# Kernel optimization log

Hardware: AMD Instinct MI355X
Metric: run time of the kernel (lower is better)

Reference implementation:

```python
import jax, jax.numpy as jnp
from jax import lax
import numpy as np

B, T, I, H = 4096, 200, 32, 6  # batch, seq_len, input_size, hidden


def _lstm_layer(x_seq, W_ih, W_hh, b_ih, b_hh):
    """Single unidirectional LSTM layer, PyTorch gate order (i,f,g,o).
    x_seq: [B,T,Din]. Returns (all_h [B,T,H], h_last [B,H])."""
    Bb = x_seq.shape[0]
    Hh = W_hh.shape[1]
    # Precompute input projections for all timesteps (hoisted out of the scan).
    x_proj = jnp.einsum('bti,gi->btg', x_seq, W_ih) + b_ih + b_hh  # [B,T,4H]

    def step(carry, xp_t):
        h, c = carry
        gates = xp_t + h @ W_hh.T  # [B,4H]
        i_g, f_g, g_g, o_g = jnp.split(gates, 4, axis=-1)
        i_g = jax.nn.sigmoid(i_g)
        f_g = jax.nn.sigmoid(f_g)
        g_g = jnp.tanh(g_g)
        o_g = jax.nn.sigmoid(o_g)
        c = f_g * c + i_g * g_g
        h = o_g * jnp.tanh(c)
        return (h, c), h

    init = (jnp.zeros((Bb, Hh), x_seq.dtype), jnp.zeros((Bb, Hh), x_seq.dtype))
    (h_last, _), hs = lax.scan(step, init, jnp.swapaxes(x_proj, 0, 1))  # time-major scan
    return jnp.swapaxes(hs, 0, 1), h_last


def setup_inputs() -> dict:
    key = jax.random.key(0)
    ks = jax.random.split(key, 11)
    s = 0.2  # ~ uniform(-1/sqrt(H)) scale for H=6
    inp = {
        'x': jax.random.normal(ks[0], (B, T, I), dtype=jnp.float32),
        'W_ih0': jax.random.normal(ks[1], (4 * H, I), dtype=jnp.float32) * s,
        'W_hh0': jax.random.normal(ks[2], (4 * H, H), dtype=jnp.float32) * s,
        'b_ih0': jax.random.normal(ks[3], (4 * H,), dtype=jnp.float32) * s,
        'b_hh0': jax.random.normal(ks[4], (4 * H,), dtype=jnp.float32) * s,
        'W_ih1': jax.random.normal(ks[5], (4 * H, H), dtype=jnp.float32) * s,
        'W_hh1': jax.random.normal(ks[6], (4 * H, H), dtype=jnp.float32) * s,
        'b_ih1': jax.random.normal(ks[7], (4 * H,), dtype=jnp.float32) * s,
        'b_hh1': jax.random.normal(ks[8], (4 * H,), dtype=jnp.float32) * s,
        'W_lin': jax.random.normal(ks[9], (1, H), dtype=jnp.float32) * s,
        'b_lin': jax.random.normal(ks[10], (1,), dtype=jnp.float32) * s,
    }
    return inp


def reference(x, W_ih0, W_hh0, b_ih0, b_hh0, W_ih1, W_hh1, b_ih1, b_hh1, W_lin, b_lin):
    # Layer 0 (eval mode: inter-layer dropout disabled)
    h1_seq, _ = _lstm_layer(x, W_ih0, W_hh0, b_ih0, b_hh0)
    # Layer 1
    _, h2_last = _lstm_layer(h1_seq, W_ih1, W_hh1, b_ih1, b_hh1)
    # Linear head on last layer's final hidden state: [B,1]
    return h2_last @ W_lin.T + b_lin
```

## Files before the change

### kernel.cpp

```cpp
#include <hip/hip_runtime.h>


#define TLEN  200
#define ISZ   32
#define HSZ   6
#define WPITCH 36

#define PWOFF 0
#define PBOFF (24 * WPITCH)
#define PLDS_DW (PBOFF + 24)

#define RPITCH 25
#define RING_DW (64 * RPITCH)
#define FWOFF  RING_DW
#define FBOFF  (FWOFF + 24 * WPITCH)
#define FLDS_DW (FBOFF + 24)

#define XP4_COUNT ((size_t)4096 * TLEN * 6)
#define WS_REQ    ((XP4_COUNT + 6) * 16)

__device__ __forceinline__ float fast_sig(float x) {
    return __builtin_amdgcn_rcpf(1.0f + __expf(-x));
}
__device__ __forceinline__ float tanh_s(float x) {
    return fmaf(2.0f, fast_sig(x + x), -1.0f);
}
__device__ __forceinline__ float rl(float v, int l) {
    return __int_as_float(__builtin_amdgcn_readlane(__float_as_int(v), l));
}
template <int CTRL>
__device__ __forceinline__ float qperm(float v) {
    return __int_as_float(__builtin_amdgcn_mov_dpp(__float_as_int(v), CTRL, 0xf, 0xf, true));
}
template <int OFF>
__device__ __forceinline__ float swz(float v) {
    return __int_as_float(__builtin_amdgcn_ds_swizzle(__float_as_int(v), OFF));
}
__device__ __forceinline__ float dot4(float4 w, float4 v) {
    return fmaf(w.x, v.x, fmaf(w.y, v.y, fmaf(w.z, v.z, w.w * v.w)));
}

__global__ __launch_bounds__(64) void proj_k(
    const float* __restrict__ x,    const float* __restrict__ Wih0,
    const float* __restrict__ bih0, const float* __restrict__ bhh0,
    const float* __restrict__ bih1, const float* __restrict__ bhh1,
    float4* __restrict__ xp4)
{
    __shared__ float lds[PLDS_DW];
    const int lane = threadIdx.x;
    const int b    = blockIdx.x;
    const int o = lane & 1;
    const int L = lane >> 1;
    const float* xb = x + (size_t)b * TLEN * ISZ;

#pragma unroll
    for (int k = 0; k < 13; ++k) {
        const int idx = lane + (k << 6);
        if (idx < 768) {
            const int row = idx >> 5, kk = idx & 31;
            const int slot = ((row % 6) / 3) * 12 + (row / 6) * 3 + (row % 3);
            lds[PWOFF + slot * WPITCH + kk] = Wih0[idx];
        } else if (idx < 792) {
            const int r = idx - 768;
            const int slot = ((r % 6) / 3) * 12 + (r / 6) * 3 + (r % 3);
            lds[PBOFF + slot] = bih0[r] + bhh0[r];
        }
    }
    if (blockIdx.x == 0 && lane < 24) {
        const int u = lane % 6, g = lane / 6;
        ((float*)(xp4 + XP4_COUNT))[u * 4 + g] = bih1[g * 6 + u] + bhh1[g * 6 + u];
    }

#define PLDSW(ROW, KCQ) (*(const float4*)&lds[PWOFF + (o * 12 + (ROW)) * WPITCH + ((KCQ) << 2)])
#pragma unroll 1
    for (int w = 0; w < 7; ++w) {
        const int t = (w << 5) + L;
        if (t < TLEN) {
            const float4* xr4 = (const float4*)(xb + (size_t)t * ISZ);
            float a0c[12];
#pragma unroll
            for (int jj = 0; jj < 12; ++jj) a0c[jj] = 0.0f;
#pragma unroll
            for (int hh = 0; hh < 2; ++hh) {
                float4 xw[4];
#pragma unroll
                for (int q = 0; q < 4; ++q) xw[q] = xr4[(hh << 2) + q];
#pragma unroll
                for (int jh = 0; jh < 2; ++jh)
#pragma unroll
                    for (int kc = 0; kc < 4; ++kc)
#pragma unroll
                        for (int jj = jh * 6; jj < jh * 6 + 6; ++jj)
                            a0c[jj] += dot4(PLDSW(jj, (hh << 2) + kc), xw[kc]);
            }
            float vv[12];
#pragma unroll
            for (int jj = 0; jj < 12; ++jj) vv[jj] = a0c[jj] + lds[PBOFF + o * 12 + jj];
            float4* dst = xp4 + ((size_t)b * TLEN + t) * 6 + 3 * o;
#pragma unroll
            for (int v = 0; v < 3; ++v)
                dst[v] = make_float4(vv[v], vv[3 + v], vv[6 + v], vv[9 + v]);
        }
    }
#undef PLDSW
}

__global__ __launch_bounds__(64) void lstm_scan(
    const float* __restrict__ Whh0, const float* __restrict__ Wih1,
    const float* __restrict__ Whh1, const float* __restrict__ Wlin,
    const float* __restrict__ blin, const float4* __restrict__ xp4,
    float* __restrict__ out)
{
    const int lane = threadIdx.x;
    const int role = lane & 15;
    const int grp  = lane >> 4;
    const int b    = blockIdx.x * 4 + grp;

    float WA[4][6], WB[4][6];
#pragma unroll
    for (int g = 0; g < 4; ++g)
#pragma unroll
        for (int k = 0; k < 6; ++k) { WA[g][k] = 0.0f; WB[g][k] = 0.0f; }
    if (role < 6) {
#pragma unroll
        for (int g = 0; g < 4; ++g)
#pragma unroll
            for (int k = 0; k < 6; ++k) WA[g][k] = Whh0[(g * 6 + role) * 6 + k];
    } else if (role < 12) {
        const int u = role - 6;
#pragma unroll
        for (int g = 0; g < 4; ++g)
#pragma unroll
            for (int k = 0; k < 6; ++k) {
                WA[g][k] = Wih1[(g * 6 + u) * 6 + k];
                WB[g][k] = Whh1[(g * 6 + u) * 6 + k];
            }
    }
    const float4* P;
    int ST;
    if (role < 6) { P = xp4 + (size_t)b * TLEN * 6 + role; ST = 6; }
    else          { P = xp4 + XP4_COUNT + (role < 12 ? role - 6 : 0); ST = 0; }

    float4 q0 = P[0], q1 = P[ST], q2 = P[2 * ST], q3 = P[3 * ST];
    P += 4 * ST;

    float c = 0.0f, h = 0.0f;

#define STEP(XQ) do { \
    const float hA0 = swz<0x010>(h), hA1 = swz<0x030>(h), hA2 = swz<0x050>(h); \
    const float hA3 = swz<0x070>(h), hA4 = swz<0x090>(h), hA5 = swz<0x0B0>(h); \
    const float hB0 = swz<0x0D0>(h), hB1 = swz<0x0F0>(h), hB2 = swz<0x110>(h); \
    const float hB3 = swz<0x130>(h), hB4 = swz<0x150>(h), hB5 = swz<0x170>(h); \
    float a0 = (XQ).x, a1 = (XQ).y, a2 = (XQ).z, a3 = (XQ).w; \
    ARG(a0, 0); ARG(a1, 1); ARG(a2, 2); ARG(a3, 3); \
    const float ig = fast_sig(a0), fg = fast_sig(a1); \
    const float gg = tanh_s(a2),   og = fast_sig(a3); \
    c = fmaf(fg, c, ig * gg); \
    h = og * tanh_s(c); \
} while (0)

#define ARG(A, G) do { \
    const float s0 = fmaf(WA[G][0], hA0, fmaf(WA[G][1], hA1, fmaf(WA[G][2], hA2, A))); \
    const float s1 = fmaf(WA[G][3], hA3, fmaf(WA[G][4], hA4, WA[G][5] * hA5)); \
    const float s2 = fmaf(WB[G][0], hB0, fmaf(WB[G][1], hB1, WB[G][2] * hB2)); \
    const float s3 = fmaf(WB[G][3], hB3, fmaf(WB[G][4], hB4, WB[G][5] * hB5)); \
    A = (s0 + s1) + (s2 + s3); \
} while (0)

#define STEPR(QV) do { const float4 _xq = QV; QV = *P; P += ST; STEP(_xq); } while (0)

    STEPR(q0);
    h = (role < 6) ? h : 0.0f;
    c = (role < 6) ? c : 0.0f;

#pragma unroll 1
    for (int m = 0; m < 48; ++m) {
        STEPR(q1); STEPR(q2); STEPR(q3); STEPR(q0);
    }
    STEPR(q1); STEPR(q2); STEPR(q3);
    STEP(q0); STEP(q1); STEP(q2); STEP(q3);
    STEP(q0);

    {
        const float f0 = swz<0x0D0>(h), f1 = swz<0x0F0>(h), f2 = swz<0x110>(h);
        const float f3 = swz<0x130>(h), f4 = swz<0x150>(h), f5 = swz<0x170>(h);
        float s = blin[0];
        s = fmaf(Wlin[0], f0, s); s = fmaf(Wlin[1], f1, s);
        s = fmaf(Wlin[2], f2, s); s = fmaf(Wlin[3], f3, s);
        s = fmaf(Wlin[4], f4, s); s = fmaf(Wlin[5], f5, s);
        if (role == 0) out[b] = s;
    }
#undef STEP
#undef ARG
#undef STEPR
}

__global__ __launch_bounds__(64) void lstm_fb(
    const float* __restrict__ x,
    const float* __restrict__ Wih0, const float* __restrict__ Whh0,
    const float* __restrict__ bih0, const float* __restrict__ bhh0,
    const float* __restrict__ Wih1, const float* __restrict__ Whh1,
    const float* __restrict__ bih1, const float* __restrict__ bhh1,
    const float* __restrict__ Wlin, const float* __restrict__ blin,
    float* __restrict__ out)
{
    __shared__ float lds[FLDS_DW];

    const int lane = threadIdx.x;
    const int b    = blockIdx.x;

    const int o = lane & 1;
    const int L = lane >> 1;

    const bool loHalf = (lane < 32);
    const int  p  = lane & 3;
    const int  jq = (lane & 31) >> 2;
    const int  j  = (jq < HSZ) ? jq : 0;
    const int  r  = 6 * p + j;

#define LDSW(ROW, KCQ) (*(const float4*)&lds[FWOFF + (o * 12 + (ROW)) * WPITCH + ((KCQ) << 2)])

#pragma unroll
    for (int k = 0; k < 13; ++k) {
        const int idx = lane + (k << 6);
        if (idx < 768) {
            const int row = idx >> 5, kk = idx & 31;
            lds[FWOFF + row * WPITCH + kk] = Wih0[idx];
        } else if (idx < 792) {
            lds[FBOFF + idx - 768] = bih0[idx - 768] + bhh0[idx - 768];
        }
    }

    float WA[6], WB[6], base1 = 0.0f, sgc = 1.0f, tgc = 0.0f;
#pragma unroll
    for (int k = 0; k < 6; ++k) { WA[k] = 0.0f; WB[k] = 0.0f; }
    if (loHalf) {
#pragma unroll
        for (int k = 0; k < 6; ++k) WA[k] = Whh0[r * 6 + k];
    } else {
#pragma unroll
        for (int k = 0; k < 6; ++k) { WA[k] = Wih1[r * 6 + k]; WB[k] = Whh1[r * 6 + k]; }
        base1 = bih1[r] + bhh1[r];
    }
    if (p == 2) {
#pragma unroll
        for (int k = 0; k < 6; ++k) { WA[k] *= 2.0f; WB[k] *= 2.0f; }
        base1 *= 2.0f; sgc = 2.0f; tgc = -1.0f;
    }

    const float* xb = x + (size_t)b * TLEN * ISZ;

#pragma unroll
    for (int w01 = 0; w01 < 2; ++w01) {
        const int t = (w01 << 5) + L;
        const float4* xr4 = (const float4*)(xb + t * ISZ);
        float4 xw[8];
#pragma unroll
        for (int q = 0; q < 8; ++q) xw[q] = xr4[q];
        float a0c[12];
#pragma unroll
        for (int jj = 0; jj < 12; ++jj) a0c[jj] = 0.0f;
#pragma unroll
        for (int kc = 0; kc < 8; ++kc)
#pragma unroll
            for (int jj = 0; jj < 12; ++jj)
                a0c[jj] += dot4(LDSW(jj, kc), xw[kc]);
#pragma unroll
        for (int jj = 0; jj < 12; ++jj) {
            float v = a0c[jj] + lds[FBOFF + o * 12 + jj];
            if (jj < 6) v = (o == 1) ? v * 2.0f : v;
            lds[t * RPITCH + o * 12 + jj] = v;
        }
    }

    float acc[12];
#pragma unroll
    for (int jj = 0; jj < 12; ++jj) acc[jj] = 0.0f;
    const float* pc = xb + (size_t)min(64 + L, TLEN - 1) * ISZ;
    const float* pn = xb + (size_t)min(96 + L, TLEN - 1) * ISZ;
    float4 f0, f1;
    f1 = *((const float4*)pc);
    float4 Wp0 = LDSW(0, 0), Wp1 = LDSW(1, 0), Wp2 = LDSW(2, 0);

    float c = 0.0f, h = 0.0f;
    float xp_cur = lds[r];

#define KC_HEAD(KC) do { \
    f0 = f1; \
    const float4* _srcp = ((KC) < 7) ? ((const float4*)pc + (KC) + 1) \
                                     : ((const float4*)pn); \
    f1 = *_srcp; \
} while (0)

#define SPREAD_STEP(RT, KC) do { \
    acc[3*(RT)+0] += dot4(Wp0, f0); \
    acc[3*(RT)+1] += dot4(Wp1, f0); \
    acc[3*(RT)+2] += dot4(Wp2, f0); \
    const int _rtn = ((RT) + 1) & 3; \
    const int _kcn = ((RT) == 3) ? (((KC) + 1) & 7) : (KC); \
    Wp0 = LDSW(3*_rtn + 0, _kcn); \
    Wp1 = LDSW(3*_rtn + 1, _kcn); \
    Wp2 = LDSW(3*_rtn + 2, _kcn); \
} while (0)

#define SCAN_STEP(ITV) do { \
    const float h10=rl(h,0),  h11=rl(h,4),  h12=rl(h,8); \
    const float h13=rl(h,12), h14=rl(h,16), h15=rl(h,20); \
    const float h20=rl(h,32), h21=rl(h,36), h22=rl(h,40); \
    const float h23=rl(h,44), h24=rl(h,48), h25=rl(h,52); \
    const float _xn = lds[(((ITV) + 1) & 63) * RPITCH + r]; \
    const float _g0 = loHalf ? xp_cur : base1; \
    const float _a0 = fmaf(WA[0],h10, fmaf(WA[2],h12, fmaf(WA[4],h14, _g0))); \
    const float _a1 = fmaf(WA[1],h11, fmaf(WA[3],h13, WA[5]*h15)); \
    const float _b0 = fmaf(WB[0],h20, fmaf(WB[2],h22, WB[4]*h24)); \
    const float _b1 = fmaf(WB[1],h21, fmaf(WB[3],h23, WB[5]*h25)); \
    const float _g  = (_a0 + _a1) + (_b0 + _b1); \
    const float _aG = fmaf(sgc, fast_sig(_g), tgc); \
    const float _iq = qperm<0x00>(_aG), _fq = qperm<0x55>(_aG); \
    const float _gq = qperm<0xAA>(_aG), _oq = qperm<0xFF>(_aG); \
    c = fmaf(_fq, c, _iq * _gq); \
    const float _th = fmaf(2.0f, fast_sig(2.0f * c), -1.0f); \
    h = _oq * _th; \
    xp_cur = _xn; \
    if ((ITV) == 200) { \
        float _s = blin[0]; \
        _s = fmaf(Wlin[0], rl(h, 32), _s); \
        _s = fmaf(Wlin[1], rl(h, 36), _s); \
        _s = fmaf(Wlin[2], rl(h, 40), _s); \
        _s = fmaf(Wlin[3], rl(h, 44), _s); \
        _s = fmaf(Wlin[4], rl(h, 48), _s); \
        _s = fmaf(Wlin[5], rl(h, 52), _s); \
        if (lane == 0) out[b] = _s; \
    } \
} while (0)

#define ENTRY(IT0) do { \
    const int _slot = ((IT0) + 32 + L) & 63; \
    _Pragma("unroll") \
    for (int _jj = 0; _jj < 12; ++_jj) { \
        float _v = acc[_jj] + lds[FBOFF + o * 12 + _jj]; \
        if (_jj < 6) _v = (o == 1) ? _v * 2.0f : _v; \
        lds[_slot * RPITCH + o * 12 + _jj] = _v; \
        acc[_jj] = 0.0f; \
    } \
    pc = pn; \
    pn = xb + (size_t)min((IT0) + 96 + L, TLEN - 1) * ISZ; \
} while (0)

    KC_HEAD(0);
    SPREAD_STEP(0, 0);
    {
        const float g  = loHalf ? xp_cur : base1;
        const float aG = fmaf(sgc, fast_sig(g), tgc);
        const float iq = qperm<0x00>(aG), gq = qperm<0xAA>(aG), oq = qperm<0xFF>(aG);
        const float cn = iq * gq;
        const float th = fmaf(2.0f, fast_sig(2.0f * cn), -1.0f);
        c = loHalf ? cn : 0.0f;
        h = loHalf ? (oq * th) : 0.0f;
        xp_cur = lds[RPITCH + r];
    }

    SPREAD_STEP(1, 0); SCAN_STEP(1);
    SPREAD_STEP(2, 0); SCAN_STEP(2);
    SPREAD_STEP(3, 0); SCAN_STEP(3);
    for (int kc = 1; kc < 8; ++kc) {
        KC_HEAD(kc);
        const int itb = kc << 2;
        SPREAD_STEP(0, kc); SCAN_STEP(itb + 0);
        SPREAD_STEP(1, kc); SCAN_STEP(itb + 1);
        SPREAD_STEP(2, kc); SCAN_STEP(itb + 2);
        SPREAD_STEP(3, kc); SCAN_STEP(itb + 3);
    }

    for (int w = 1; w < 7; ++w) {
        const int it0 = w << 5;
        ENTRY(it0);
        for (int kc = 0; kc < 8; ++kc) {
            const int itb = it0 + (kc << 2);
            if (itb > 200) break;
            KC_HEAD(kc);
            SPREAD_STEP(0, kc); SCAN_STEP(itb + 0);
            SPREAD_STEP(1, kc); SCAN_STEP(itb + 1);
            SPREAD_STEP(2, kc); SCAN_STEP(itb + 2);
            SPREAD_STEP(3, kc); SCAN_STEP(itb + 3);
        }
    }

#undef LDSW
#undef KC_HEAD
#undef SPREAD_STEP
#undef SCAN_STEP
#undef ENTRY
}

extern "C" void kernel_launch(void* const* d_in, const int* in_sizes, int n_in,
                              void* d_out, int out_size, void* d_ws, size_t ws_size,
                              hipStream_t stream) {
    const float* x    = (const float*)d_in[0];
    const float* Wih0 = (const float*)d_in[1];
    const float* Whh0 = (const float*)d_in[2];
    const float* bih0 = (const float*)d_in[3];
    const float* bhh0 = (const float*)d_in[4];
    const float* Wih1 = (const float*)d_in[5];
    const float* Whh1 = (const float*)d_in[6];
    const float* bih1 = (const float*)d_in[7];
    const float* bhh1 = (const float*)d_in[8];
    const float* Wlin = (const float*)d_in[9];
    const float* blin = (const float*)d_in[10];
    float* out = (float*)d_out;

    if (d_ws != nullptr && ws_size >= WS_REQ) {
        float4* xp4 = (float4*)d_ws;
        proj_k<<<4096, 64, 0, stream>>>(x, Wih0, bih0, bhh0, bih1, bhh1, xp4);
        lstm_scan<<<1024, 64, 0, stream>>>(Whh0, Wih1, Whh1, Wlin, blin,
                                           (const float4*)xp4, out);
    } else {
        lstm_fb<<<4096, 64, 0, stream>>>(x, Wih0, Whh0, bih0, bhh0,
                                         Wih1, Whh1, bih1, bhh1,
                                         Wlin, blin, out);
    }
}
```

Measured before the change: 253.2 us.

## Flatten projection to one row per thread; use DPP row rotates in scan

The input projection kernel now gives each thread a single (batch,time) row, with weights read straight from global/constant memory instead of an LDS-staged layout, over 12800 blocks. The scan kernel swaps the 12 ds_swizzle broadcasts per step for 15 DPP row-rotates, with weights pre-permuted per lane so each lane does 16 FMAs per gate. The aim is to cut LDS-path latency on the serial recurrence and simplify projection scheduling. The cost is more FMAs per step and heavier register use, and the projection now relies on scalar weight loads.

```diff
diff --git a/kernel.cpp b/kernel.cpp
--- a/kernel.cpp
+++ b/kernel.cpp
@@ -5,10 +5,6 @@
 #define ISZ   32
 #define HSZ   6
 #define WPITCH 36
-
-#define PWOFF 0
-#define PBOFF (24 * WPITCH)
-#define PLDS_DW (PBOFF + 24)
 
 #define RPITCH 25
 #define RING_DW (64 * RPITCH)
@@ -36,76 +32,54 @@
 __device__ __forceinline__ float swz(float v) {
     return __int_as_float(__builtin_amdgcn_ds_swizzle(__float_as_int(v), OFF));
 }
+template <int M>
+__device__ __forceinline__ float rotf(float v) {
+    return __int_as_float(__builtin_amdgcn_mov_dpp(__float_as_int(v), 0x120 + M, 0xf, 0xf, true));
+}
 __device__ __forceinline__ float dot4(float4 w, float4 v) {
     return fmaf(w.x, v.x, fmaf(w.y, v.y, fmaf(w.z, v.z, w.w * v.w)));
 }
 
-__global__ __launch_bounds__(64) void proj_k(
+__global__ __launch_bounds__(64) void proj_k2(
     const float* __restrict__ x,    const float* __restrict__ Wih0,
     const float* __restrict__ bih0, const float* __restrict__ bhh0,
     const float* __restrict__ bih1, const float* __restrict__ bhh1,
     float4* __restrict__ xp4)
 {
-    __shared__ float lds[PLDS_DW];
     const int lane = threadIdx.x;
-    const int b    = blockIdx.x;
-    const int o = lane & 1;
-    const int L = lane >> 1;
-    const float* xb = x + (size_t)b * TLEN * ISZ;
-
-#pragma unroll
-    for (int k = 0; k < 13; ++k) {
-        const int idx = lane + (k << 6);
-        if (idx < 768) {
-            const int row = idx >> 5, kk = idx & 31;
-            const int slot = ((row % 6) / 3) * 12 + (row / 6) * 3 + (row % 3);
-            lds[PWOFF + slot * WPITCH + kk] = Wih0[idx];
-        } else if (idx < 792) {
-            const int r = idx - 768;
-            const int slot = ((r % 6) / 3) * 12 + (r / 6) * 3 + (r % 3);
-            lds[PBOFF + slot] = bih0[r] + bhh0[r];
-        }
-    }
+    const size_t n = (size_t)blockIdx.x * 64 + lane;
+
     if (blockIdx.x == 0 && lane < 24) {
         const int u = lane % 6, g = lane / 6;
         ((float*)(xp4 + XP4_COUNT))[u * 4 + g] = bih1[g * 6 + u] + bhh1[g * 6 + u];
     }
 
-#define PLDSW(ROW, KCQ) (*(const float4*)&lds[PWOFF + (o * 12 + (ROW)) * WPITCH + ((KCQ) << 2)])
-#pragma unroll 1
-    for (int w = 0; w < 7; ++w) {
-        const int t = (w << 5) + L;
-        if (t < TLEN) {
-            const float4* xr4 = (const float4*)(xb + (size_t)t * ISZ);
-            float a0c[12];
-#pragma unroll
-            for (int jj = 0; jj < 12; ++jj) a0c[jj] = 0.0f;
-#pragma unroll
-            for (int hh = 0; hh < 2; ++hh) {
-                float4 xw[4];
-#pragma unroll
-                for (int q = 0; q < 4; ++q) xw[q] = xr4[(hh << 2) + q];
-#pragma unroll
-                for (int jh = 0; jh < 2; ++jh)
-#pragma unroll
-                    for (int kc = 0; kc < 4; ++kc)
-#pragma unroll
-                        for (int jj = jh * 6; jj < jh * 6 + 6; ++jj)
-                            a0c[jj] += dot4(PLDSW(jj, (hh << 2) + kc), xw[kc]);
-            }
-            float vv[12];
-#pragma unroll
-            for (int jj = 0; jj < 12; ++jj) vv[jj] = a0c[jj] + lds[PBOFF + o * 12 + jj];
-            float4* dst = xp4 + ((size_t)b * TLEN + t) * 6 + 3 * o;
-#pragma unroll
-            for (int v = 0; v < 3; ++v)
-                dst[v] = make_float4(vv[v], vv[3 + v], vv[6 + v], vv[9 + v]);
+    const float4* xr = (const float4*)(x + n * ISZ);
+    float4 xv[8];
+#pragma unroll
+    for (int q = 0; q < 8; ++q) xv[q] = xr[q];
+
+    float acc[24];
+#pragma unroll
+    for (int r = 0; r < 24; ++r) {
+        float a = bih0[r] + bhh0[r];
+        const float* wr = Wih0 + r * ISZ;
+#pragma unroll
+        for (int q = 0; q < 8; ++q) {
+            a = fmaf(wr[q * 4 + 0], xv[q].x, a);
+            a = fmaf(wr[q * 4 + 1], xv[q].y, a);
+            a = fmaf(wr[q * 4 + 2], xv[q].z, a);
+            a = fmaf(wr[q * 4 + 3], xv[q].w, a);
         }
-    }
-#undef PLDSW
-}
-
-__global__ __launch_bounds__(64) void lstm_scan(
+        acc[r] = a;
+    }
+    float4* dst = xp4 + n * 6;
+#pragma unroll
+    for (int u = 0; u < 6; ++u)
+        dst[u] = make_float4(acc[u], acc[6 + u], acc[12 + u], acc[18 + u]);
+}
+
+__global__ __launch_bounds__(64) void scan_k3(
     const float* __restrict__ Whh0, const float* __restrict__ Wih1,
     const float* __restrict__ Whh1, const float* __restrict__ Wlin,
     const float* __restrict__ blin, const float4* __restrict__ xp4,
@@ -116,26 +90,31 @@
     const int grp  = lane >> 4;
     const int b    = blockIdx.x * 4 + grp;
 
-    float WA[4][6], WB[4][6];
+    int sr[16];
+    sr[0] = role;
+#define PRB(M) sr[M] = __builtin_amdgcn_mov_dpp(lane, 0x120 + M, 0xf, 0xf, true) & 15;
+    PRB(1)  PRB(2)  PRB(3)  PRB(4)  PRB(5)  PRB(6)  PRB(7)
+    PRB(8)  PRB(9)  PRB(10) PRB(11) PRB(12) PRB(13) PRB(14) PRB(15)
+#undef PRB
+
+    const int lt = (role < 6) ? 0 : (role < 12 ? 1 : 2);
+    const int u  = (role < 6) ? role : (role < 12 ? role - 6 : 0);
+    float Wq[4][16];
 #pragma unroll
     for (int g = 0; g < 4; ++g)
 #pragma unroll
-        for (int k = 0; k < 6; ++k) { WA[g][k] = 0.0f; WB[g][k] = 0.0f; }
-    if (role < 6) {
-#pragma unroll
-        for (int g = 0; g < 4; ++g)
-#pragma unroll
-            for (int k = 0; k < 6; ++k) WA[g][k] = Whh0[(g * 6 + role) * 6 + k];
-    } else if (role < 12) {
-        const int u = role - 6;
-#pragma unroll
-        for (int g = 0; g < 4; ++g)
-#pragma unroll
-            for (int k = 0; k < 6; ++k) {
-                WA[g][k] = Wih1[(g * 6 + u) * 6 + k];
-                WB[g][k] = Whh1[(g * 6 + u) * 6 + k];
+        for (int m = 0; m < 16; ++m) {
+            const int s = sr[m];
+            float w = 0.0f;
+            if (lt == 0) {
+                if (s < 6) w = Whh0[(g * 6 + u) * 6 + s];
+            } else if (lt == 1) {
+                if (s < 6)       w = Wih1[(g * 6 + u) * 6 + s];
+                else if (s < 12) w = Whh1[(g * 6 + u) * 6 + (s - 6)];
             }
-    }
+            Wq[g][m] = w;
+        }
+
     const float4* P;
     int ST;
     if (role < 6) { P = xp4 + (size_t)b * TLEN * 6 + role; ST = 6; }
@@ -146,25 +125,38 @@
 
     float c = 0.0f, h = 0.0f;
 
+#define GATE(G, BASE) ({ \
+    float _s0 = fmaf(Wq[G][0], h, (BASE)); \
+    _s0 = fmaf(Wq[G][2],  hm2,  _s0); \
+    _s0 = fmaf(Wq[G][4],  hm4,  _s0); \
+    _s0 = fmaf(Wq[G][6],  hm6,  _s0); \
+    _s0 = fmaf(Wq[G][8],  hm8,  _s0); \
+    _s0 = fmaf(Wq[G][10], hm10, _s0); \
+    _s0 = fmaf(Wq[G][12], hm12, _s0); \
+    _s0 = fmaf(Wq[G][14], hm14, _s0); \
+    float _s1 = fmaf(Wq[G][1], hm1, Wq[G][3] * hm3); \
+    _s1 = fmaf(Wq[G][5],  hm5,  _s1); \
+    _s1 = fmaf(Wq[G][7],  hm7,  _s1); \
+    _s1 = fmaf(Wq[G][9],  hm9,  _s1); \
+    _s1 = fmaf(Wq[G][11], hm11, _s1); \
+    _s1 = fmaf(Wq[G][13], hm13, _s1); \
+    _s1 = fmaf(Wq[G][15], hm15, _s1); \
+    _s0 + _s1; })
+
 #define STEP(XQ) do { \
-    const float hA0 = swz<0x010>(h), hA1 = swz<0x030>(h), hA2 = swz<0x050>(h); \
-    const float hA3 = swz<0x070>(h), hA4 = swz<0x090>(h), hA5 = swz<0x0B0>(h); \
-    const float hB0 = swz<0x0D0>(h), hB1 = swz<0x0F0>(h), hB2 = swz<0x110>(h); \
-    const float hB3 = swz<0x130>(h), hB4 = swz<0x150>(h), hB5 = swz<0x170>(h); \
-    float a0 = (XQ).x, a1 = (XQ).y, a2 = (XQ).z, a3 = (XQ).w; \
-    ARG(a0, 0); ARG(a1, 1); ARG(a2, 2); ARG(a3, 3); \
-    const float ig = fast_sig(a0), fg = fast_sig(a1); \
-    const float gg = tanh_s(a2),   og = fast_sig(a3); \
+    const float hm1 = rotf<1>(h),   hm2 = rotf<2>(h),   hm3 = rotf<3>(h); \
+    const float hm4 = rotf<4>(h),   hm5 = rotf<5>(h),   hm6 = rotf<6>(h); \
+    const float hm7 = rotf<7>(h),   hm8 = rotf<8>(h),   hm9 = rotf<9>(h); \
+    const float hm10 = rotf<10>(h), hm11 = rotf<11>(h), hm12 = rotf<12>(h); \
+    const float hm13 = rotf<13>(h), hm14 = rotf<14>(h), hm15 = rotf<15>(h); \
+    const float A0 = GATE(0, (XQ).x); \
+    const float A1 = GATE(1, (XQ).y); \
+    const float A2 = GATE(2, (XQ).z); \
+    const float A3 = GATE(3, (XQ).w); \
+    const float ig = fast_sig(A0), fg = fast_sig(A1); \
+    const float gg = tanh_s(A2),   og = fast_sig(A3); \
     c = fmaf(fg, c, ig * gg); \
     h = og * tanh_s(c); \
-} while (0)
-
-#define ARG(A, G) do { \
-    const float s0 = fmaf(WA[G][0], hA0, fmaf(WA[G][1], hA1, fmaf(WA[G][2], hA2, A))); \
-    const float s1 = fmaf(WA[G][3], hA3, fmaf(WA[G][4], hA4, WA[G][5] * hA5)); \
-    const float s2 = fmaf(WB[G][0], hB0, fmaf(WB[G][1], hB1, WB[G][2] * hB2)); \
-    const float s3 = fmaf(WB[G][3], hB3, fmaf(WB[G][4], hB4, WB[G][5] * hB5)); \
-    A = (s0 + s1) + (s2 + s3); \
 } while (0)
 
 #define STEPR(QV) do { const float4 _xq = QV; QV = *P; P += ST; STEP(_xq); } while (0)
@@ -191,8 +183,8 @@
         if (role == 0) out[b] = s;
     }
 #undef STEP
-#undef ARG
 #undef STEPR
+#undef GATE
 }
 
 __global__ __launch_bounds__(64) void lstm_fb(
@@ -411,9 +403,9 @@
 
     if (d_ws != nullptr && ws_size >= WS_REQ) {
         float4* xp4 = (float4*)d_ws;
-        proj_k<<<4096, 64, 0, stream>>>(x, Wih0, bih0, bhh0, bih1, bhh1, xp4);
-        lstm_scan<<<1024, 64, 0, stream>>>(Whh0, Wih1, Whh1, Wlin, blin,
-                                           (const float4*)xp4, out);
+        proj_k2<<<12800, 64, 0, stream>>>(x, Wih0, bih0, bhh0, bih1, bhh1, xp4);
+        scan_k3<<<1024, 64, 0, stream>>>(Whh0, Wih1, Whh1, Wlin, blin,
+                                         (const float4*)xp4, out);
     } else {
         lstm_fb<<<4096, 64, 0, stream>>>(x, Wih0, Whh0, bih0, bhh0,
                                          Wih1, Whh1, bih1, bhh1,
```

After: 291.3 us. 15.1% more time.

## Restructure projection kernel per-gate with LDS-staged x, halve scan batches per wave

Applied to the files above, without the earlier changes.

The projection kernel now assigns one gate row per lane and keeps its 32 input weights in registers. It stages 64 timesteps of x into LDS and has two lane groups handle alternating timesteps, writing scalar outputs in the interleaved layout. This replaces the old version, which read weights from LDS and had each lane compute 12 gates. The scan kernel now packs only 2 batch elements per 64-lane wave instead of 4 and launches twice as many blocks, aiming for more waves and latency hiding at the cost of half-idle lanes. The projection stores become scattered 4-byte writes, and a quarter of its lanes do no work.

```diff
diff --git a/kernel.cpp b/kernel.cpp
--- a/kernel.cpp
+++ b/kernel.cpp
@@ -5,10 +5,6 @@
 #define ISZ   32
 #define HSZ   6
 #define WPITCH 36
-
-#define PWOFF 0
-#define PBOFF (24 * WPITCH)
-#define PLDS_DW (PBOFF + 24)
 
 #define RPITCH 25
 #define RING_DW (64 * RPITCH)
@@ -40,72 +36,69 @@
     return fmaf(w.x, v.x, fmaf(w.y, v.y, fmaf(w.z, v.z, w.w * v.w)));
 }
 
-__global__ __launch_bounds__(64) void proj_k(
+__global__ __launch_bounds__(64) void proj_k3(
     const float* __restrict__ x,    const float* __restrict__ Wih0,
     const float* __restrict__ bih0, const float* __restrict__ bhh0,
     const float* __restrict__ bih1, const float* __restrict__ bhh1,
     float4* __restrict__ xp4)
 {
-    __shared__ float lds[PLDS_DW];
+    __shared__ float xs[64 * 36];
+
     const int lane = threadIdx.x;
     const int b    = blockIdx.x;
-    const int o = lane & 1;
-    const int L = lane >> 1;
     const float* xb = x + (size_t)b * TLEN * ISZ;
 
-#pragma unroll
-    for (int k = 0; k < 13; ++k) {
-        const int idx = lane + (k << 6);
-        if (idx < 768) {
-            const int row = idx >> 5, kk = idx & 31;
-            const int slot = ((row % 6) / 3) * 12 + (row / 6) * 3 + (row % 3);
-            lds[PWOFF + slot * WPITCH + kk] = Wih0[idx];
-        } else if (idx < 792) {
-            const int r = idx - 768;
-            const int slot = ((r % 6) / 3) * 12 + (r / 6) * 3 + (r % 3);
-            lds[PBOFF + slot] = bih0[r] + bhh0[r];
-        }
-    }
-    if (blockIdx.x == 0 && lane < 24) {
+    if (b == 0 && lane < 24) {
         const int u = lane % 6, g = lane / 6;
         ((float*)(xp4 + XP4_COUNT))[u * 4 + g] = bih1[g * 6 + u] + bhh1[g * 6 + u];
     }
 
-#define PLDSW(ROW, KCQ) (*(const float4*)&lds[PWOFF + (o * 12 + (ROW)) * WPITCH + ((KCQ) << 2)])
+    const int s  = lane / 24;
+    const int se = (s == 2) ? 0 : s;
+    const int g  = lane - s * 24;
+    const bool act = (lane < 48);
+
+    float4 w4[8];
+    const float4* wr = (const float4*)(Wih0 + g * ISZ);
+#pragma unroll
+    for (int q = 0; q < 8; ++q) w4[q] = wr[q];
+    const float bg = bih0[g] + bhh0[g];
+
+    const int ofs = (g % 6) * 4 + g / 6;
+    float* xpb = (float*)(xp4 + (size_t)b * TLEN * 6);
+
 #pragma unroll 1
-    for (int w = 0; w < 7; ++w) {
-        const int t = (w << 5) + L;
-        if (t < TLEN) {
-            const float4* xr4 = (const float4*)(xb + (size_t)t * ISZ);
-            float a0c[12];
-#pragma unroll
-            for (int jj = 0; jj < 12; ++jj) a0c[jj] = 0.0f;
-#pragma unroll
-            for (int hh = 0; hh < 2; ++hh) {
-                float4 xw[4];
-#pragma unroll
-                for (int q = 0; q < 4; ++q) xw[q] = xr4[(hh << 2) + q];
-#pragma unroll
-                for (int jh = 0; jh < 2; ++jh)
-#pragma unroll
-                    for (int kc = 0; kc < 4; ++kc)
-#pragma unroll
-                        for (int jj = jh * 6; jj < jh * 6 + 6; ++jj)
-                            a0c[jj] += dot4(PLDSW(jj, (hh << 2) + kc), xw[kc]);
+    for (int tc = 0; tc < TLEN; tc += 64) {
+        const int nrows = (TLEN - tc >= 64) ? 64 : (TLEN - tc);
+        const float4* src = (const float4*)(xb + (size_t)tc * ISZ);
+        for (int f = lane; f < nrows * 8; f += 64) {
+            const int row = f >> 3, kq = f & 7;
+            *(float4*)&xs[row * 36 + kq * 4] = src[f];
+        }
+        const int half = nrows >> 1;
+#pragma unroll 1
+        for (int i = 0; i < half; ++i) {
+            const int rr = 2 * i + se;
+            float a0 = bg, a1 = 0.0f;
+#pragma unroll
+            for (int q = 0; q < 4; ++q) {
+                const float4 xv = *(const float4*)&xs[rr * 36 + q * 4];
+                a0 = fmaf(w4[q].x, xv.x, a0); a0 = fmaf(w4[q].y, xv.y, a0);
+                a0 = fmaf(w4[q].z, xv.z, a0); a0 = fmaf(w4[q].w, xv.w, a0);
             }
-            float vv[12];
-#pragma unroll
-            for (int jj = 0; jj < 12; ++jj) vv[jj] = a0c[jj] + lds[PBOFF + o * 12 + jj];
-            float4* dst = xp4 + ((size_t)b * TLEN + t) * 6 + 3 * o;
-#pragma unroll
-            for (int v = 0; v < 3; ++v)
-                dst[v] = make_float4(vv[v], vv[3 + v], vv[6 + v], vv[9 + v]);
+#pragma unroll
+            for (int q = 4; q < 8; ++q) {
+                const float4 xv = *(const float4*)&xs[rr * 36 + q * 4];
+                a1 = fmaf(w4[q].x, xv.x, a1); a1 = fmaf(w4[q].y, xv.y, a1);
+                a1 = fmaf(w4[q].z, xv.z, a1); a1 = fmaf(w4[q].w, xv.w, a1);
+            }
+            const float a = a0 + a1;
+            if (act) xpb[(size_t)(tc + rr) * 24 + ofs] = a;
         }
     }
-#undef PLDSW
-}
-
-__global__ __launch_bounds__(64) void lstm_scan(
+}
+
+__global__ __launch_bounds__(64) void scan_k4(
     const float* __restrict__ Whh0, const float* __restrict__ Wih1,
     const float* __restrict__ Whh1, const float* __restrict__ Wlin,
     const float* __restrict__ blin, const float4* __restrict__ xp4,
@@ -114,37 +107,47 @@
     const int lane = threadIdx.x;
     const int role = lane & 15;
     const int grp  = lane >> 4;
-    const int b    = blockIdx.x * 4 + grp;
+    const bool act = (grp < 2);
+    const int b    = blockIdx.x * 2 + (grp & 1);
 
     float WA[4][6], WB[4][6];
 #pragma unroll
-    for (int g = 0; g < 4; ++g)
-#pragma unroll
-        for (int k = 0; k < 6; ++k) { WA[g][k] = 0.0f; WB[g][k] = 0.0f; }
-    if (role < 6) {
-#pragma unroll
-        for (int g = 0; g < 4; ++g)
-#pragma unroll
-            for (int k = 0; k < 6; ++k) WA[g][k] = Whh0[(g * 6 + role) * 6 + k];
-    } else if (role < 12) {
+    for (int gg = 0; gg < 4; ++gg)
+#pragma unroll
+        for (int k = 0; k < 6; ++k) { WA[gg][k] = 0.0f; WB[gg][k] = 0.0f; }
+    if (act && role < 6) {
+#pragma unroll
+        for (int gg = 0; gg < 4; ++gg)
+#pragma unroll
+            for (int k = 0; k < 6; ++k) WA[gg][k] = Whh0[(gg * 6 + role) * 6 + k];
+    } else if (act && role < 12) {
         const int u = role - 6;
 #pragma unroll
-        for (int g = 0; g < 4; ++g)
+        for (int gg = 0; gg < 4; ++gg)
 #pragma unroll
             for (int k = 0; k < 6; ++k) {
-                WA[g][k] = Wih1[(g * 6 + u) * 6 + k];
-                WB[g][k] = Whh1[(g * 6 + u) * 6 + k];
+                WA[gg][k] = Wih1[(gg * 6 + u) * 6 + k];
+                WB[gg][k] = Whh1[(gg * 6 + u) * 6 + k];
             }
     }
+
     const float4* P;
     int ST;
-    if (role < 6) { P = xp4 + (size_t)b * TLEN * 6 + role; ST = 6; }
-    else          { P = xp4 + XP4_COUNT + (role < 12 ? role - 6 : 0); ST = 0; }
+    if (act && role < 6) { P = xp4 + (size_t)b * TLEN * 6 + role; ST = 6; }
+    else { P = xp4 + XP4_COUNT + ((role >= 6 && role < 12) ? role - 6 : 0); ST = 0; }
 
     float4 q0 = P[0], q1 = P[ST], q2 = P[2 * ST], q3 = P[3 * ST];
     P += 4 * ST;
 
     float c = 0.0f, h = 0.0f;
+
+#define ARG(A, G) do { \
+    const float s0 = fmaf(WA[G][0], hA0, fmaf(WA[G][1], hA1, fmaf(WA[G][2], hA2, A))); \
+    const float s1 = fmaf(WA[G][3], hA3, fmaf(WA[G][4], hA4, WA[G][5] * hA5)); \
+    const float s2 = fmaf(WB[G][0], hB0, fmaf(WB[G][1], hB1, WB[G][2] * hB2)); \
+    const float s3 = fmaf(WB[G][3], hB3, fmaf(WB[G][4], hB4, WB[G][5] * hB5)); \
+    A = (s0 + s1) + (s2 + s3); \
+} while (0)
 
 #define STEP(XQ) do { \
     const float hA0 = swz<0x010>(h), hA1 = swz<0x030>(h), hA2 = swz<0x050>(h); \
@@ -159,14 +162,6 @@
     h = og * tanh_s(c); \
 } while (0)
 
-#define ARG(A, G) do { \
-    const float s0 = fmaf(WA[G][0], hA0, fmaf(WA[G][1], hA1, fmaf(WA[G][2], hA2, A))); \
-    const float s1 = fmaf(WA[G][3], hA3, fmaf(WA[G][4], hA4, WA[G][5] * hA5)); \
-    const float s2 = fmaf(WB[G][0], hB0, fmaf(WB[G][1], hB1, WB[G][2] * hB2)); \
-    const float s3 = fmaf(WB[G][3], hB3, fmaf(WB[G][4], hB4, WB[G][5] * hB5)); \
-    A = (s0 + s1) + (s2 + s3); \
-} while (0)
-
 #define STEPR(QV) do { const float4 _xq = QV; QV = *P; P += ST; STEP(_xq); } while (0)
 
     STEPR(q0);
@@ -184,15 +179,15 @@
     {
         const float f0 = swz<0x0D0>(h), f1 = swz<0x0F0>(h), f2 = swz<0x110>(h);
         const float f3 = swz<0x130>(h), f4 = swz<0x150>(h), f5 = swz<0x170>(h);
-        float s = blin[0];
-        s = fmaf(Wlin[0], f0, s); s = fmaf(Wlin[1], f1, s);
-        s = fmaf(Wlin[2], f2, s); s = fmaf(Wlin[3], f3, s);
-        s = fmaf(Wlin[4], f4, s); s = fmaf(Wlin[5], f5, s);
-        if (role == 0) out[b] = s;
+        float sOut = blin[0];
+        sOut = fmaf(Wlin[0], f0, sOut); sOut = fmaf(Wlin[1], f1, sOut);
+        sOut = fmaf(Wlin[2], f2, sOut); sOut = fmaf(Wlin[3], f3, sOut);
+        sOut = fmaf(Wlin[4], f4, sOut); sOut = fmaf(Wlin[5], f5, sOut);
+        if (act && role == 0) out[b] = sOut;
     }
 #undef STEP
+#undef STEPR
 #undef ARG
-#undef STEPR
 }
 
 __global__ __launch_bounds__(64) void lstm_fb(
@@ -411,9 +406,9 @@
 
     if (d_ws != nullptr && ws_size >= WS_REQ) {
         float4* xp4 = (float4*)d_ws;
-        proj_k<<<4096, 64, 0, stream>>>(x, Wih0, bih0, bhh0, bih1, bhh1, xp4);
-        lstm_scan<<<1024, 64, 0, stream>>>(Whh0, Wih1, Whh1, Wlin, blin,
-                                           (const float4*)xp4, out);
+        proj_k3<<<4096, 64, 0, stream>>>(x, Wih0, bih0, bhh0, bih1, bhh1, xp4);
+        scan_k4<<<2048, 64, 0, stream>>>(Whh0, Wih1, Whh1, Wlin, blin,
+                                         (const float4*)xp4, out);
     } else {
         lstm_fb<<<4096, 64, 0, stream>>>(x, Wih0, Whh0, bih0, bhh0,
                                          Wih1, Whh1, bih1, bhh1,
```

Measured after the change: 274.3 us. 8.3% more time.
